# Performance work log

Hardware: AMD Instinct MI355X
Metric: run time of the kernel (lower is better)

The kernel has to match this reference:

```python
import jax, jax.numpy as jnp
import numpy as np

B, T, D = 1, 4096, 1024
H = 16
HEAD_DIM = D // H
WINDOW = 256


def setup_inputs() -> dict:
    key = jax.random.key(0)
    k1, k2, k3 = jax.random.split(key, 3)
    x = jax.random.normal(k1, (B, T, D), dtype=jnp.float32)
    # torch nn.Linear(D, 3D) weight is (3D, D); we store transposed (D, 3D) for x @ W
    w_qkv = jax.random.normal(k2, (D, 3 * D), dtype=jnp.float32) * (1.0 / np.sqrt(D))
    w_out = jax.random.normal(k3, (D, D), dtype=jnp.float32) * (1.0 / np.sqrt(D))
    return {"x": x, "w_qkv": w_qkv, "w_out": w_out}


def reference(x, w_qkv, w_out):
    b, t, d = x.shape
    qkv = x @ w_qkv                                   # (B, T, 3D)
    q, k, v = jnp.split(qkv, 3, axis=-1)
    def split_heads(a):                               # (B, T, D) -> (B, H, T, dh)
        return a.reshape(b, t, H, HEAD_DIM).transpose(0, 2, 1, 3)
    q, k, v = split_heads(q), split_heads(k), split_heads(v)
    scale = jnp.sqrt(jnp.float32(HEAD_DIM))
    scores = jnp.einsum('bhqd,bhkd->bhqk', q, k) / scale   # (B, H, T, T)
    rows = jnp.arange(t)[:, None]
    cols = jnp.arange(t)[None, :]
    # causal sliding window: j <= i and j >= i - window + 1
    mask = (cols <= rows) & (cols >= rows - WINDOW + 1)     # (T, T) bool
    scores = jnp.where(mask[None, None], scores, -jnp.inf)
    attn = jax.nn.softmax(scores, axis=-1)
    out = jnp.einsum('bhqk,bhkd->bhqd', attn, v)            # (B, H, T, dh)
    out = out.transpose(0, 2, 1, 3).reshape(b, t, d)        # merge heads
    return out @ w_out
```

## Files before the change

kernel.cpp:

```cpp
#include <hip/hip_runtime.h>
#include <hip/hip_bf16.h>

#define T_SEQ 4096
#define DMODEL 1024
#define NH 16
#define DH 64
#define N_QKV 3072
#define N_QK 2048

typedef __attribute__((ext_vector_type(8))) short bf16x8;
typedef __attribute__((ext_vector_type(4))) float f32x4;

__device__ inline void gload_lds16(const __hip_bfloat16* g, __hip_bfloat16* l) {
  __builtin_amdgcn_global_load_lds(
      (const __attribute__((address_space(1))) void*)g,
      (__attribute__((address_space(3))) void*)l, 16, 0, 0);
}

__global__ void prep_kernel(const float* __restrict__ x,
                            const float* __restrict__ w_qkv,
                            const float* __restrict__ w_out,
                            __hip_bfloat16* __restrict__ x_bf,
                            __hip_bfloat16* __restrict__ wqkvT,
                            __hip_bfloat16* __restrict__ woutT) {
  __shared__ float tile[32][33];
  const int b = blockIdx.x;
  if (b < 4096) {
    int i = (b * 256 + threadIdx.x) * 4;
    float4 v = *(const float4*)(x + i);
    ushort4 o;
    o.x = __bfloat16_as_ushort(__float2bfloat16(v.x));
    o.y = __bfloat16_as_ushort(__float2bfloat16(v.y));
    o.z = __bfloat16_as_ushort(__float2bfloat16(v.z));
    o.w = __bfloat16_as_ushort(__float2bfloat16(v.w));
    *(ushort4*)((unsigned short*)x_bf + i) = o;
    return;
  }
  const float* in;
  __hip_bfloat16* out;
  int NN, KK, bn, bk;
  if (b < 7168) {
    int idx = b - 4096;
    in = w_qkv; out = wqkvT; NN = N_QKV; KK = DMODEL;
    bn = (idx % 96) * 32; bk = (idx / 96) * 32;
  } else {
    int idx = b - 7168;
    in = w_out; out = woutT; NN = DMODEL; KK = DMODEL;
    bn = (idx % 32) * 32; bk = (idx / 32) * 32;
  }
  int tx = threadIdx.x & 31, ty = threadIdx.x >> 5;
#pragma unroll
  for (int r = 0; r < 32; r += 8)
    tile[ty + r][tx] = in[(size_t)(bk + ty + r) * NN + bn + tx];
  __syncthreads();
#pragma unroll
  for (int r = 0; r < 32; r += 8)
    out[(size_t)(bn + ty + r) * KK + bk + tx] = __float2bfloat16(tile[tx][ty + r]);
}

__global__ __launch_bounds__(512, 2) void gemm8_qkv(
    const __hip_bfloat16* __restrict__ A, const __hip_bfloat16* __restrict__ Bt,
    __hip_bfloat16* __restrict__ qk, __hip_bfloat16* __restrict__ vt) {
  const int K = DMODEL;
  __shared__ alignas(16) __hip_bfloat16 Ab[3][256 * 64];
  __shared__ alignas(16) __hip_bfloat16 Bb[2][192 * 64];

  const int tid = threadIdx.x;
  const int lane = tid & 63;
  const int w = tid >> 6;
  const int wr = w >> 2, wc = w & 3;
  const int frow = lane & 15, fgrp = lane >> 4;

  const int bid = blockIdx.x;
  const int sbid = (bid & 7) * 32 + (bid >> 3);
  const int mb = sbid >> 4, nb = sbid & 15;
  const int brow = mb << 8, bcol = nb * 192;

  const int srow = lane >> 3;
  const int sslot = (lane & 7) ^ srow;
  const __hip_bfloat16* aSrcA = A + (size_t)(brow + w * 32 + srow) * K + sslot * 8;
  const __hip_bfloat16* aSrcB = Bt + (size_t)(bcol + w * 24 + srow) * K + sslot * 8;
  const int dstA = (w * 32 + srow) * 64 + (lane & 7) * 8;
  const int dstB = (w * 24 + srow) * 64 + (lane & 7) * 8;

  f32x4 acc[8][3] = {};

#pragma unroll
  for (int i = 0; i < 4; i++)
    gload_lds16(aSrcA + (size_t)(i * 8) * K, &Ab[0][dstA + i * 8 * 64]);
#pragma unroll
  for (int i = 0; i < 3; i++)
    gload_lds16(aSrcB + (size_t)(i * 8) * K, &Bb[0][dstB + i * 8 * 64]);
#pragma unroll
  for (int i = 0; i < 4; i++)
    gload_lds16(aSrcA + (size_t)(i * 8) * K + 64, &Ab[1][dstA + i * 8 * 64]);

  for (int t = 0; t < 16; ++t) {
    if (t < 15)
      asm volatile("s_waitcnt vmcnt(4)" ::: "memory");
    else
      asm volatile("s_waitcnt vmcnt(0)" ::: "memory");
    __builtin_amdgcn_s_barrier();

    const __hip_bfloat16* As = &Ab[t % 3][0];
    const __hip_bfloat16* Bs = &Bb[t & 1][0];
    bf16x8 bfrag[3][2], afrag[4][2];

#pragma unroll
    for (int n = 0; n < 3; n++) {
      int row = wc * 48 + n * 16 + frow;
#pragma unroll
      for (int kh = 0; kh < 2; kh++) {
        int slot = (kh * 4 + fgrp) ^ (row & 7);
        bfrag[n][kh] = *(const bf16x8*)(Bs + row * 64 + slot * 8);
      }
    }
#pragma unroll
    for (int m = 0; m < 4; m++) {
      int row = wr * 128 + m * 16 + frow;
#pragma unroll
      for (int kh = 0; kh < 2; kh++) {
        int slot = (kh * 4 + fgrp) ^ (row & 7);
        afrag[m][kh] = *(const bf16x8*)(As + row * 64 + slot * 8);
      }
    }
    if (t + 1 < 16) {
      __hip_bfloat16* bd = &Bb[(t + 1) & 1][0];
#pragma unroll
      for (int i = 0; i < 3; i++)
        gload_lds16(aSrcB + (size_t)(i * 8) * K + (t + 1) * 64, bd + dstB + i * 8 * 64);
    }
    __builtin_amdgcn_s_barrier();
    __builtin_amdgcn_s_setprio(1);
#pragma unroll
    for (int m = 0; m < 4; m++)
#pragma unroll
      for (int n = 0; n < 3; n++) {
        acc[m][n] = __builtin_amdgcn_mfma_f32_16x16x32_bf16(afrag[m][0], bfrag[n][0], acc[m][n], 0, 0, 0);
        acc[m][n] = __builtin_amdgcn_mfma_f32_16x16x32_bf16(afrag[m][1], bfrag[n][1], acc[m][n], 0, 0, 0);
      }
    __builtin_amdgcn_s_setprio(0);
    __builtin_amdgcn_s_barrier();

#pragma unroll
    for (int m = 0; m < 4; m++) {
      int row = wr * 128 + (m + 4) * 16 + frow;
#pragma unroll
      for (int kh = 0; kh < 2; kh++) {
        int slot = (kh * 4 + fgrp) ^ (row & 7);
        afrag[m][kh] = *(const bf16x8*)(As + row * 64 + slot * 8);
      }
    }
    if (t + 2 < 16) {
      __hip_bfloat16* ad = &Ab[(t + 2) % 3][0];
#pragma unroll
      for (int i = 0; i < 4; i++)
        gload_lds16(aSrcA + (size_t)(i * 8) * K + (t + 2) * 64, ad + dstA + i * 8 * 64);
    }
    __builtin_amdgcn_s_barrier();
    __builtin_amdgcn_s_setprio(1);
#pragma unroll
    for (int m = 0; m < 4; m++)
#pragma unroll
      for (int n = 0; n < 3; n++) {
        acc[m + 4][n] = __builtin_amdgcn_mfma_f32_16x16x32_bf16(afrag[m][0], bfrag[n][0], acc[m + 4][n], 0, 0, 0);
        acc[m + 4][n] = __builtin_amdgcn_mfma_f32_16x16x32_bf16(afrag[m][1], bfrag[n][1], acc[m + 4][n], 0, 0, 0);
      }
    __builtin_amdgcn_s_setprio(0);
  }

  const int orow0 = brow + wr * 128 + 4 * fgrp;
  const int ocol0 = bcol + wc * 48 + frow;
#pragma unroll
  for (int m = 0; m < 8; m++)
#pragma unroll
    for (int n = 0; n < 3; n++) {
      int col = ocol0 + n * 16;
      int row0 = orow0 + m * 16;
      if (col < N_QK) {
        float sc = (col < DMODEL) ? 0.125f : 1.0f;
#pragma unroll
        for (int j = 0; j < 4; j++)
          qk[(size_t)(row0 + j) * N_QK + col] = __float2bfloat16(acc[m][n][j] * sc);
      } else {
        ushort4 pack;
        pack.x = __bfloat16_as_ushort(__float2bfloat16(acc[m][n][0]));
        pack.y = __bfloat16_as_ushort(__float2bfloat16(acc[m][n][1]));
        pack.z = __bfloat16_as_ushort(__float2bfloat16(acc[m][n][2]));
        pack.w = __bfloat16_as_ushort(__float2bfloat16(acc[m][n][3]));
        *(ushort4*)((unsigned short*)vt + (size_t)(col - N_QK) * T_SEQ + row0) = pack;
      }
    }
}

__global__ __launch_bounds__(256) void gemm_out(
    const __hip_bfloat16* __restrict__ A, const __hip_bfloat16* __restrict__ Bt,
    float* __restrict__ C) {
  const int K = DMODEL, N = DMODEL;
  __shared__ alignas(16) __hip_bfloat16 Ab[4][128 * 32];
  __shared__ alignas(16) __hip_bfloat16 Bb[4][128 * 32];
  const int tid = threadIdx.x, lane = tid & 63, w = tid >> 6;
  const int wr = w >> 1, wc = w & 1;
  const int frow = lane & 15, fgrp = lane >> 4;
  const int bid = blockIdx.x;
  const int sbid = (bid & 7) * 32 + (bid >> 3);
  const int mb = sbid >> 3, nb = sbid & 7;
  const int brow = mb * 128, bcol = nb * 128;

  const int sr = tid >> 2;
  const int swz = ((tid & 3) ^ ((sr >> 1) & 3)) << 3;
  const __hip_bfloat16* aA = A + (size_t)(brow + sr) * K + swz;
  const __hip_bfloat16* aB = Bt + (size_t)(bcol + sr) * K + swz;
  const int dlo = sr * 32 + (tid & 3) * 8;
  const int dhi = (sr + 64) * 32 + (tid & 3) * 8;

  f32x4 acc[4][4] = {};
#pragma unroll
  for (int t = 0; t < 3; t++) {
    gload_lds16(aA + t * 32, &Ab[t][dlo]);
    gload_lds16(aA + 64 * (size_t)K + t * 32, &Ab[t][dhi]);
    gload_lds16(aB + t * 32, &Bb[t][dlo]);
    gload_lds16(aB + 64 * (size_t)K + t * 32, &Bb[t][dhi]);
  }
  for (int t = 0; t < 32; ++t) {
    if (t < 30)
      asm volatile("s_waitcnt vmcnt(8)" ::: "memory");
    else if (t == 30)
      asm volatile("s_waitcnt vmcnt(4)" ::: "memory");
    else
      asm volatile("s_waitcnt vmcnt(0)" ::: "memory");
    __builtin_amdgcn_s_barrier();
    const __hip_bfloat16* As = Ab[t & 3];
    const __hip_bfloat16* Bs = Bb[t & 3];
    if (t + 3 < 32) {
      gload_lds16(aA + (t + 3) * 32, &Ab[(t + 3) & 3][dlo]);
      gload_lds16(aA + 64 * (size_t)K + (t + 3) * 32, &Ab[(t + 3) & 3][dhi]);
      gload_lds16(aB + (t + 3) * 32, &Bb[(t + 3) & 3][dlo]);
      gload_lds16(aB + 64 * (size_t)K + (t + 3) * 32, &Bb[(t + 3) & 3][dhi]);
    }
    bf16x8 af[4], bfr[4];
#pragma unroll
    for (int m = 0; m < 4; m++) {
      int row = wr * 64 + m * 16 + frow;
      af[m] = *(const bf16x8*)(As + row * 32 + ((fgrp ^ ((row >> 1) & 3)) << 3));
    }
#pragma unroll
    for (int n = 0; n < 4; n++) {
      int row = wc * 64 + n * 16 + frow;
      bfr[n] = *(const bf16x8*)(Bs + row * 32 + ((fgrp ^ ((row >> 1) & 3)) << 3));
    }
    __builtin_amdgcn_s_barrier();
    __builtin_amdgcn_s_setprio(1);
#pragma unroll
    for (int m = 0; m < 4; m++)
#pragma unroll
      for (int n = 0; n < 4; n++)
        acc[m][n] = __builtin_amdgcn_mfma_f32_16x16x32_bf16(af[m], bfr[n], acc[m][n], 0, 0, 0);
    __builtin_amdgcn_s_setprio(0);
  }
  const int orow0 = brow + wr * 64 + 4 * fgrp;
  const int ocol0 = bcol + wc * 64 + frow;
#pragma unroll
  for (int m = 0; m < 4; m++)
#pragma unroll
    for (int n = 0; n < 4; n++)
#pragma unroll
      for (int j = 0; j < 4; j++)
        C[(size_t)(orow0 + m * 16 + j) * N + ocol0 + n * 16] = acc[m][n][j];
}

__global__ __launch_bounds__(256) void swa_kernel(
    const __hip_bfloat16* __restrict__ qk, const __hip_bfloat16* __restrict__ vt,
    __hip_bfloat16* __restrict__ attn_out) {
  const int b = blockIdx.x;
  const int s = (b & 7) * 128 + (b >> 3);
  const int h = s >> 6;
  const int qb = s & 63;
  const int tid = threadIdx.x;
  const int lane = tid & 63;
  const int w = tid >> 6;
  const int frow = lane & 15;
  const int fgrp = lane >> 4;
  const int fk = fgrp * 8;

  __shared__ alignas(16) __hip_bfloat16 Ks[2][64 * 64];
  __shared__ alignas(16) __hip_bfloat16 Vs[64 * 64];
  __shared__ alignas(16) __hip_bfloat16 Pl[4][16 * 72];

  const int qrow_g = qb * 64 + w * 16 + frow;
  bf16x8 aq[2];
  {
    const __hip_bfloat16* qptr = qk + (size_t)qrow_g * N_QK + h * DH;
    aq[0] = *(const bf16x8*)(qptr + fk);
    aq[1] = *(const bf16x8*)(qptr + 32 + fk);
  }

  f32x4 o[4] = {};
  float l_run[4] = {0.f, 0.f, 0.f, 0.f};

  const int srow = lane >> 3;
  const int ssw = (((lane & 7) ^ srow) << 3);
  const __hip_bfloat16* kbase =
      qk + (size_t)(w * 16 + srow) * N_QK + DMODEL + h * DH + ssw;
  const __hip_bfloat16* vbase =
      vt + (size_t)(h * DH + w * 16 + srow) * T_SEQ + ssw;

  const int kb0 = qb >= 4 ? qb - 4 : 0;

  {
    const __hip_bfloat16* ks = kbase + (size_t)kb0 * 64 * N_QK;
    gload_lds16(ks, &Ks[0][w * 16 * 64]);
    gload_lds16(ks + 8 * (size_t)N_QK, &Ks[0][(w * 16 + 8) * 64]);
  }

  for (int kb = kb0; kb <= qb; kb++) {
    const int buf = (kb - kb0) & 1;
    {
      const __hip_bfloat16* vs = vbase + kb * 64;
      gload_lds16(vs, &Vs[w * 16 * 64]);
      gload_lds16(vs + 8 * (size_t)T_SEQ, &Vs[(w * 16 + 8) * 64]);
    }
    if (kb < qb) {
      const __hip_bfloat16* ks = kbase + (size_t)(kb + 1) * 64 * N_QK;
      gload_lds16(ks, &Ks[buf ^ 1][w * 16 * 64]);
      gload_lds16(ks + 8 * (size_t)N_QK, &Ks[buf ^ 1][(w * 16 + 8) * 64]);
      asm volatile("s_waitcnt vmcnt(4)" ::: "memory");
    } else {
      asm volatile("s_waitcnt vmcnt(2)" ::: "memory");
    }
    __builtin_amdgcn_s_barrier();

    f32x4 sc[4];
#pragma unroll
    for (int n = 0; n < 4; n++) sc[n] = (f32x4){0.f, 0.f, 0.f, 0.f};
#pragma unroll
    for (int n = 0; n < 4; n++) {
      int rowk = n * 16 + frow;
      int x = rowk & 7;
      bf16x8 bk0 = *(const bf16x8*)(&Ks[buf][rowk * 64 + ((fgrp ^ x) << 3)]);
      bf16x8 bk1 = *(const bf16x8*)(&Ks[buf][rowk * 64 + (((4 + fgrp) ^ x) << 3)]);
      sc[n] = __builtin_amdgcn_mfma_f32_16x16x32_bf16(aq[0], bk0, sc[n], 0, 0, 0);
      sc[n] = __builtin_amdgcn_mfma_f32_16x16x32_bf16(aq[1], bk1, sc[n], 0, 0, 0);
    }

    const bool edge_hi = (kb == qb);
    const bool edge_lo = (kb == qb - 4);
#pragma unroll
    for (int r = 0; r < 4; r++) {
      const int row_l = w * 16 + 4 * fgrp + r;
      float rs = 0.f;
#pragma unroll
      for (int n = 0; n < 4; n++) {
        int col_l = n * 16 + frow;
        bool valid = (!edge_hi || col_l <= row_l) && (!edge_lo || col_l > row_l);
        float p = valid ? __expf(sc[n][r]) : 0.f;
        sc[n][r] = p;
        rs += p;
      }
      l_run[r] += rs;
    }

    __hip_bfloat16* pw = &Pl[w][0];
#pragma unroll
    for (int n = 0; n < 4; n++)
#pragma unroll
      for (int r = 0; r < 4; r++)
        pw[(4 * fgrp + r) * 72 + n * 16 + frow] = __float2bfloat16(sc[n][r]);

    if (kb < qb)
      asm volatile("s_waitcnt vmcnt(2)" ::: "memory");
    else
      asm volatile("s_waitcnt vmcnt(0)" ::: "memory");
    __builtin_amdgcn_s_barrier();

#pragma unroll
    for (int c = 0; c < 2; c++) {
      bf16x8 ap = *(const bf16x8*)(pw + frow * 72 + c * 32 + fk);
#pragma unroll
      for (int nd = 0; nd < 4; nd++) {
        int rowd = nd * 16 + frow;
        int x = rowd & 7;
        bf16x8 bv = *(const bf16x8*)(&Vs[rowd * 64 + (((c * 4 + fgrp) ^ x) << 3)]);
        o[nd] = __builtin_amdgcn_mfma_f32_16x16x32_bf16(ap, bv, o[nd], 0, 0, 0);
      }
    }
    __builtin_amdgcn_s_barrier();
  }

  float linv[4];
#pragma unroll
  for (int r = 0; r < 4; r++) {
    float l = l_run[r];
    l += __shfl_xor(l, 1);
    l += __shfl_xor(l, 2);
    l += __shfl_xor(l, 4);
    l += __shfl_xor(l, 8);
    linv[r] = 1.0f / l;
  }
#pragma unroll
  for (int nd = 0; nd < 4; nd++)
#pragma unroll
    for (int r = 0; r < 4; r++) {
      float v = o[nd][r] * linv[r];
      attn_out[(size_t)(qb * 64 + w * 16 + 4 * fgrp + r) * DMODEL + h * DH + nd * 16 + frow] =
          __float2bfloat16(v);
    }
}

extern "C" void kernel_launch(void* const* d_in, const int* in_sizes, int n_in,
                              void* d_out, int out_size, void* d_ws, size_t ws_size,
                              hipStream_t stream) {
  const float* x = (const float*)d_in[0];
  const float* w_qkv = (const float*)d_in[1];
  const float* w_out = (const float*)d_in[2];
  float* out = (float*)d_out;

  char* ws = (char*)d_ws;
  __hip_bfloat16* x_bf = (__hip_bfloat16*)ws;
  __hip_bfloat16* wqkvT = (__hip_bfloat16*)(ws + 8388608);
  __hip_bfloat16* woutT = (__hip_bfloat16*)(ws + 14680064);
  __hip_bfloat16* qk_bf = (__hip_bfloat16*)(ws + 16777216);
  __hip_bfloat16* vt = (__hip_bfloat16*)(ws + 33554432);
  __hip_bfloat16* attn_bf = (__hip_bfloat16*)(ws + 41943040);

  prep_kernel<<<8192, 256, 0, stream>>>(x, w_qkv, w_out, x_bf, wqkvT, woutT);

  gemm8_qkv<<<(T_SEQ / 256) * (N_QKV / 192), 512, 0, stream>>>(x_bf, wqkvT, qk_bf, vt);

  swa_kernel<<<(T_SEQ / 64) * NH, 256, 0, stream>>>(qk_bf, vt, attn_bf);

  gemm_out<<<256, 256, 0, stream>>>(attn_bf, woutT, out);
}
```

Measured before the change: 80.75 us.

## Retile QKV GEMM to 256x256 blocks with quadrant-staged 4-slot LDS pipeline

The QKV projection GEMM now uses 256x256 output tiles (192 blocks instead of 256) in place of 256x192. A and B are each staged as two 128-row halves into a 4-slot LDS ring, and each k-step runs as four quadrant MMA phases that interleave the next step's half-tile loads. Per-warp fragment mapping and the epilogue indexing change to match. The intent is more MFMA work per LDS byte and finer overlap of loads with compute, at the cost of more accumulator registers (8x4 tiles) and fewer blocks than CUs for load balance.

New measurement: 92.97 us. 15.1% more time.

```diff
diff --git a/kernel.cpp b/kernel.cpp
--- a/kernel.cpp
+++ b/kernel.cpp
@@ -62,8 +62,8 @@
     const __hip_bfloat16* __restrict__ A, const __hip_bfloat16* __restrict__ Bt,
     __hip_bfloat16* __restrict__ qk, __hip_bfloat16* __restrict__ vt) {
   const int K = DMODEL;
-  __shared__ alignas(16) __hip_bfloat16 Ab[3][256 * 64];
-  __shared__ alignas(16) __hip_bfloat16 Bb[2][192 * 64];
+  __shared__ alignas(16) __hip_bfloat16 Ab[4][128 * 64];
+  __shared__ alignas(16) __hip_bfloat16 Bb[4][128 * 64];
 
   const int tid = threadIdx.x;
   const int lane = tid & 63;
@@ -72,125 +72,144 @@
   const int frow = lane & 15, fgrp = lane >> 4;
 
   const int bid = blockIdx.x;
-  const int sbid = (bid & 7) * 32 + (bid >> 3);
-  const int mb = sbid >> 4, nb = sbid & 15;
-  const int brow = mb << 8, bcol = nb * 192;
-
-  const int srow = lane >> 3;
-  const int sslot = (lane & 7) ^ srow;
-  const __hip_bfloat16* aSrcA = A + (size_t)(brow + w * 32 + srow) * K + sslot * 8;
-  const __hip_bfloat16* aSrcB = Bt + (size_t)(bcol + w * 24 + srow) * K + sslot * 8;
-  const int dstA = (w * 32 + srow) * 64 + (lane & 7) * 8;
-  const int dstB = (w * 24 + srow) * 64 + (lane & 7) * 8;
-
-  f32x4 acc[8][3] = {};
-
-#pragma unroll
-  for (int i = 0; i < 4; i++)
-    gload_lds16(aSrcA + (size_t)(i * 8) * K, &Ab[0][dstA + i * 8 * 64]);
-#pragma unroll
-  for (int i = 0; i < 3; i++)
-    gload_lds16(aSrcB + (size_t)(i * 8) * K, &Bb[0][dstB + i * 8 * 64]);
-#pragma unroll
-  for (int i = 0; i < 4; i++)
-    gload_lds16(aSrcA + (size_t)(i * 8) * K + 64, &Ab[1][dstA + i * 8 * 64]);
+  const int sbid = (bid & 7) * 24 + (bid >> 3);
+  const int mb = sbid / 12, nb = sbid % 12;
+  const int brow = mb << 8, bcol = nb << 8;
+
+  const int srow = tid >> 3;
+  const int sslot = (tid & 7) ^ (srow & 7);
+  const __hip_bfloat16* aSrcA = A + (size_t)(brow + srow) * K + sslot * 8;
+  const __hip_bfloat16* aSrcB = Bt + (size_t)(bcol + srow) * K + sslot * 8;
+  const int dstOff = srow * 64 + (tid & 7) * 8;
+
+#define STG_A(t, h)                                                              \
+  do {                                                                           \
+    int _sl = (2 * (t) + (h)) & 3;                                               \
+    gload_lds16(aSrcA + (size_t)((h)*128) * K + (t)*64, &Ab[_sl][dstOff]);       \
+    gload_lds16(aSrcA + (size_t)((h)*128 + 64) * K + (t)*64,                     \
+                &Ab[_sl][4096 + dstOff]);                                        \
+  } while (0)
+#define STG_B(t, h)                                                              \
+  do {                                                                           \
+    int _sl = (2 * (t) + (h)) & 3;                                               \
+    gload_lds16(aSrcB + (size_t)((h)*128) * K + (t)*64, &Bb[_sl][dstOff]);       \
+    gload_lds16(aSrcB + (size_t)((h)*128 + 64) * K + (t)*64,                     \
+                &Bb[_sl][4096 + dstOff]);                                        \
+  } while (0)
+
+  f32x4 acc[8][4] = {};
+  bf16x8 afr[4][2], bfr[2][2];
+  const int rsw = frow & 7;
+
+#define READ_A(qm, t)                                                            \
+  do {                                                                           \
+    const __hip_bfloat16* _as = &Ab[(2 * (t) + (qm)) & 3][0];                    \
+    _Pragma("unroll") for (int m = 0; m < 4; m++) {                              \
+      int loc = m * 32 + wr * 16 + frow;                                         \
+      _Pragma("unroll") for (int kh = 0; kh < 2; kh++)                           \
+          afr[m][kh] =                                                           \
+          *(const bf16x8*)(_as + loc * 64 + (((kh * 4 + fgrp) ^ rsw) << 3));     \
+    }                                                                            \
+  } while (0)
+#define READ_B(qn, t)                                                            \
+  do {                                                                           \
+    const __hip_bfloat16* _bs = &Bb[(2 * (t) + (qn)) & 3][0];                    \
+    _Pragma("unroll") for (int n = 0; n < 2; n++) {                              \
+      int loc = n * 64 + wc * 16 + frow;                                         \
+      _Pragma("unroll") for (int kh = 0; kh < 2; kh++)                           \
+          bfr[n][kh] =                                                           \
+          *(const bf16x8*)(_bs + loc * 64 + (((kh * 4 + fgrp) ^ rsw) << 3));     \
+    }                                                                            \
+  } while (0)
+#define MMA(qm, qn)                                                              \
+  do {                                                                           \
+    __builtin_amdgcn_s_setprio(1);                                               \
+    _Pragma("unroll") for (int m = 0; m < 4; m++)                                \
+        _Pragma("unroll") for (int n = 0; n < 2; n++)                            \
+            _Pragma("unroll") for (int kh = 0; kh < 2; kh++)                     \
+                acc[(qm)*4 + m][(qn)*2 + n] =                                    \
+        __builtin_amdgcn_mfma_f32_16x16x32_bf16(                                 \
+            afr[m][kh], bfr[n][kh], acc[(qm)*4 + m][(qn)*2 + n], 0, 0, 0);       \
+    __builtin_amdgcn_s_setprio(0);                                               \
+  } while (0)
+
+  STG_A(0, 0);
+  STG_B(0, 0);
+  STG_A(0, 1);
+  STG_B(0, 1);
+  asm volatile("s_waitcnt vmcnt(4)" ::: "memory");
+  __builtin_amdgcn_s_barrier();
 
   for (int t = 0; t < 16; ++t) {
-    if (t < 15)
+    READ_B(0, t);
+    READ_A(0, t);
+    if (t < 15) {
+      STG_A(t + 1, 0);
       asm volatile("s_waitcnt vmcnt(4)" ::: "memory");
-    else
+    } else {
+      asm volatile("s_waitcnt vmcnt(2)" ::: "memory");
+    }
+    __builtin_amdgcn_s_barrier();
+    asm volatile("s_waitcnt lgkmcnt(0)" ::: "memory");
+    MMA(0, 0);
+    __builtin_amdgcn_s_barrier();
+
+    READ_A(1, t);
+    if (t < 15) {
+      STG_B(t + 1, 0);
+      asm volatile("s_waitcnt vmcnt(4)" ::: "memory");
+    } else {
       asm volatile("s_waitcnt vmcnt(0)" ::: "memory");
-    __builtin_amdgcn_s_barrier();
-
-    const __hip_bfloat16* As = &Ab[t % 3][0];
-    const __hip_bfloat16* Bs = &Bb[t & 1][0];
-    bf16x8 bfrag[3][2], afrag[4][2];
-
-#pragma unroll
-    for (int n = 0; n < 3; n++) {
-      int row = wc * 48 + n * 16 + frow;
-#pragma unroll
-      for (int kh = 0; kh < 2; kh++) {
-        int slot = (kh * 4 + fgrp) ^ (row & 7);
-        bfrag[n][kh] = *(const bf16x8*)(Bs + row * 64 + slot * 8);
-      }
-    }
-#pragma unroll
-    for (int m = 0; m < 4; m++) {
-      int row = wr * 128 + m * 16 + frow;
-#pragma unroll
-      for (int kh = 0; kh < 2; kh++) {
-        int slot = (kh * 4 + fgrp) ^ (row & 7);
-        afrag[m][kh] = *(const bf16x8*)(As + row * 64 + slot * 8);
-      }
-    }
-    if (t + 1 < 16) {
-      __hip_bfloat16* bd = &Bb[(t + 1) & 1][0];
-#pragma unroll
-      for (int i = 0; i < 3; i++)
-        gload_lds16(aSrcB + (size_t)(i * 8) * K + (t + 1) * 64, bd + dstB + i * 8 * 64);
-    }
-    __builtin_amdgcn_s_barrier();
-    __builtin_amdgcn_s_setprio(1);
-#pragma unroll
-    for (int m = 0; m < 4; m++)
-#pragma unroll
-      for (int n = 0; n < 3; n++) {
-        acc[m][n] = __builtin_amdgcn_mfma_f32_16x16x32_bf16(afrag[m][0], bfrag[n][0], acc[m][n], 0, 0, 0);
-        acc[m][n] = __builtin_amdgcn_mfma_f32_16x16x32_bf16(afrag[m][1], bfrag[n][1], acc[m][n], 0, 0, 0);
-      }
-    __builtin_amdgcn_s_setprio(0);
-    __builtin_amdgcn_s_barrier();
-
-#pragma unroll
-    for (int m = 0; m < 4; m++) {
-      int row = wr * 128 + (m + 4) * 16 + frow;
-#pragma unroll
-      for (int kh = 0; kh < 2; kh++) {
-        int slot = (kh * 4 + fgrp) ^ (row & 7);
-        afrag[m][kh] = *(const bf16x8*)(As + row * 64 + slot * 8);
-      }
-    }
-    if (t + 2 < 16) {
-      __hip_bfloat16* ad = &Ab[(t + 2) % 3][0];
-#pragma unroll
-      for (int i = 0; i < 4; i++)
-        gload_lds16(aSrcA + (size_t)(i * 8) * K + (t + 2) * 64, ad + dstA + i * 8 * 64);
-    }
-    __builtin_amdgcn_s_barrier();
-    __builtin_amdgcn_s_setprio(1);
-#pragma unroll
-    for (int m = 0; m < 4; m++)
-#pragma unroll
-      for (int n = 0; n < 3; n++) {
-        acc[m + 4][n] = __builtin_amdgcn_mfma_f32_16x16x32_bf16(afrag[m][0], bfrag[n][0], acc[m + 4][n], 0, 0, 0);
-        acc[m + 4][n] = __builtin_amdgcn_mfma_f32_16x16x32_bf16(afrag[m][1], bfrag[n][1], acc[m + 4][n], 0, 0, 0);
-      }
-    __builtin_amdgcn_s_setprio(0);
-  }
-
-  const int orow0 = brow + wr * 128 + 4 * fgrp;
-  const int ocol0 = bcol + wc * 48 + frow;
-#pragma unroll
-  for (int m = 0; m < 8; m++)
-#pragma unroll
-    for (int n = 0; n < 3; n++) {
-      int col = ocol0 + n * 16;
-      int row0 = orow0 + m * 16;
+    }
+    __builtin_amdgcn_s_barrier();
+    asm volatile("s_waitcnt lgkmcnt(0)" ::: "memory");
+    MMA(1, 0);
+    __builtin_amdgcn_s_barrier();
+
+    READ_B(1, t);
+    READ_A(0, t);
+    if (t < 15) STG_A(t + 1, 1);
+    __builtin_amdgcn_s_barrier();
+    asm volatile("s_waitcnt lgkmcnt(0)" ::: "memory");
+    MMA(0, 1);
+    __builtin_amdgcn_s_barrier();
+
+    READ_A(1, t);
+    if (t < 15) {
+      STG_B(t + 1, 1);
+      asm volatile("s_waitcnt vmcnt(4)" ::: "memory");
+    }
+    __builtin_amdgcn_s_barrier();
+    asm volatile("s_waitcnt lgkmcnt(0)" ::: "memory");
+    MMA(1, 1);
+    __builtin_amdgcn_s_barrier();
+  }
+
+#pragma unroll
+  for (int mm = 0; mm < 8; mm++)
+#pragma unroll
+    for (int nn = 0; nn < 4; nn++) {
+      int col = bcol + nn * 64 + wc * 16 + frow;
+      int row0 = brow + mm * 32 + wr * 16 + fgrp * 4;
       if (col < N_QK) {
         float sc = (col < DMODEL) ? 0.125f : 1.0f;
 #pragma unroll
         for (int j = 0; j < 4; j++)
-          qk[(size_t)(row0 + j) * N_QK + col] = __float2bfloat16(acc[m][n][j] * sc);
+          qk[(size_t)(row0 + j) * N_QK + col] = __float2bfloat16(acc[mm][nn][j] * sc);
       } else {
         ushort4 pack;
-        pack.x = __bfloat16_as_ushort(__float2bfloat16(acc[m][n][0]));
-        pack.y = __bfloat16_as_ushort(__float2bfloat16(acc[m][n][1]));
-        pack.z = __bfloat16_as_ushort(__float2bfloat16(acc[m][n][2]));
-        pack.w = __bfloat16_as_ushort(__float2bfloat16(acc[m][n][3]));
+        pack.x = __bfloat16_as_ushort(__float2bfloat16(acc[mm][nn][0]));
+        pack.y = __bfloat16_as_ushort(__float2bfloat16(acc[mm][nn][1]));
+        pack.z = __bfloat16_as_ushort(__float2bfloat16(acc[mm][nn][2]));
+        pack.w = __bfloat16_as_ushort(__float2bfloat16(acc[mm][nn][3]));
         *(ushort4*)((unsigned short*)vt + (size_t)(col - N_QK) * T_SEQ + row0) = pack;
       }
     }
+#undef STG_A
+#undef STG_B
+#undef READ_A
+#undef READ_B
+#undef MMA
 }
 
 __global__ __launch_bounds__(256) void gemm_out(
@@ -425,7 +444,7 @@
 
   prep_kernel<<<8192, 256, 0, stream>>>(x, w_qkv, w_out, x_bf, wqkvT, woutT);
 
-  gemm8_qkv<<<(T_SEQ / 256) * (N_QKV / 192), 512, 0, stream>>>(x_bf, wqkvT, qk_bf, vt);
+  gemm8_qkv<<<(T_SEQ / 256) * (N_QKV / 256), 512, 0, stream>>>(x_bf, wqkvT, qk_bf, vt);
 
   swa_kernel<<<(T_SEQ / 64) * NH, 256, 0, stream>>>(qk_bf, vt, attn_bf);
 
```
